# Kernel tuning notes

Measured on AMD Instinct MI355X. Metric: run time of the kernel, lower is better.

The kernel has to match this reference:

```python
import jax, jax.numpy as jnp
import numpy as np

H = 512

def setup_inputs() -> dict:
    key = jax.random.key(0)
    k1, k2, k3, k4, k5 = jax.random.split(key, 5)
    S, B = 2048, 64
    stdv = 1.0 / np.sqrt(H)
    sent_batch = jax.random.normal(k1, (S, B, H), dtype=jnp.float32)
    mean_sent_batch = jax.random.normal(k2, (B, H), dtype=jnp.float32)
    batch_mask = jnp.ones((S, B), dtype=jnp.float32)
    W = jax.random.uniform(k3, (H, H), minval=-stdv, maxval=stdv, dtype=jnp.float32)
    W_h = jax.random.uniform(k4, (H, H), minval=-stdv, maxval=stdv, dtype=jnp.float32)
    context = jax.random.uniform(k5, (H,), minval=-stdv, maxval=stdv, dtype=jnp.float32)
    return {"sent_batch": sent_batch, "mean_sent_batch": mean_sent_batch,
            "batch_mask": batch_mask, "W": W, "W_h": W_h, "context": context}


def reference(sent_batch, mean_sent_batch, batch_mask, W, W_h, context):
    # masked inputs, moved to batch-major: (B, S, H)
    r = (batch_mask[:, :, None] * sent_batch).transpose(1, 0, 2)
    WY = jnp.einsum('bsh,hk->bsk', r, W)                 # (B, S, H)
    WR = mean_sent_batch @ W_h                            # (B, H)
    M = jnp.tanh(WY + WR[:, None, :])                     # (B, S, H)
    scores = jnp.einsum('bsh,h->bs', M, context)          # (B, S)
    alpha = jax.nn.softmax(scores, axis=1)                # softmax over seq_len
    out = jnp.einsum('bs,bsh->bh', alpha, r)              # (B, H)
    return out
```

## Files before the change

kernel.cpp:

```cpp
#include <hip/hip_runtime.h>
#include <hip/hip_bf16.h>
#include <stdint.h>

#define H 512
#define SEQ 2048
#define BATCH 64
#define BH (BATCH * H)

typedef float f32x4 __attribute__((ext_vector_type(4)));
typedef short bf16x8 __attribute__((ext_vector_type(8)));

__device__ __forceinline__ unsigned short f2bf(float f) {
    unsigned int u = __float_as_uint(f);
    u += 0x7fff + ((u >> 16) & 1);
    return (unsigned short)(u >> 16);
}

__global__ __launch_bounds__(256) void prep_kernel(const float* __restrict__ W,
                                                   const float* __restrict__ mean_sb,
                                                   const float* __restrict__ W_h,
                                                   unsigned short* __restrict__ W_t,
                                                   float* __restrict__ WR) {
    int bid = blockIdx.x;
    int tid = threadIdx.x;
    if (bid < 1024) {
        int idx = bid * 256 + tid;
        int k = idx >> 9;
        int n = idx & 511;
        W_t[n * H + k] = f2bf(W[k * H + n]);
    } else {
        int b = bid - 1024;
        float a0 = 0.f, a1 = 0.f;
        for (int k = 0; k < H; ++k) {
            float m = mean_sb[b * H + k];
            a0 += m * W_h[k * H + tid];
            a1 += m * W_h[k * H + tid + 256];
        }
        WR[b * H + tid] = a0;
        WR[b * H + tid + 256] = a1;
    }
}

__global__ __launch_bounds__(256) void scores_kernel(const float* __restrict__ sent,
                                                     const float* __restrict__ mask,
                                                     const unsigned short* __restrict__ W_t,
                                                     const float* __restrict__ WR,
                                                     const float* __restrict__ ctx,
                                                     float* __restrict__ scores) {
    __shared__ uint4 A_lds[64 * 64];
    const int b = blockIdx.y;
    const int s0 = blockIdx.x * 64;
    const int tid = threadIdx.x;
    const int wave = tid >> 6;
    const int lane = tid & 63;
    const int lg = lane >> 4;
    const int ln = lane & 15;

    #pragma unroll 4
    for (int pass = 0; pass < 16; ++pass) {
        int row = pass * 4 + wave;
        int c = lane;
        const float* src = sent + (size_t)(s0 + row) * BH + b * H + c * 8;
        float4 f0 = *(const float4*)src;
        float4 f1 = *(const float4*)(src + 4);
        float m = mask[(s0 + row) * BATCH + b];
        union { unsigned short h[8]; uint4 v; } u;
        u.h[0] = f2bf(f0.x * m); u.h[1] = f2bf(f0.y * m);
        u.h[2] = f2bf(f0.z * m); u.h[3] = f2bf(f0.w * m);
        u.h[4] = f2bf(f1.x * m); u.h[5] = f2bf(f1.y * m);
        u.h[6] = f2bf(f1.z * m); u.h[7] = f2bf(f1.w * m);
        A_lds[row * 64 + (c ^ (row & 7))] = u.v;
    }
    __syncthreads();

    float p[4][4];
    #pragma unroll
    for (int m = 0; m < 4; ++m)
        #pragma unroll
        for (int r = 0; r < 4; ++r) p[m][r] = 0.f;

    const int n_wave = wave * 128;

    #pragma unroll 1
    for (int half = 0; half < 2; ++half) {
        const int n0 = n_wave + half * 64;
        f32x4 acc[4][4];
        #pragma unroll
        for (int m = 0; m < 4; ++m)
            #pragma unroll
            for (int q = 0; q < 4; ++q) acc[m][q] = (f32x4){0.f, 0.f, 0.f, 0.f};

        int arow[4], arowx[4];
        const unsigned short* wbase[4];
        #pragma unroll
        for (int m = 0; m < 4; ++m) {
            int row = m * 16 + ln;
            arow[m] = row * 64;
            arowx[m] = row & 7;
        }
        #pragma unroll
        for (int q = 0; q < 4; ++q)
            wbase[q] = W_t + (size_t)(n0 + q * 16 + ln) * H + lg * 8;

        #pragma unroll 2
        for (int ks = 0; ks < 16; ++ks) {
            bf16x8 a[4], bq[4];
            #pragma unroll
            for (int m = 0; m < 4; ++m) {
                uint4 raw = A_lds[arow[m] + ((4 * ks + lg) ^ arowx[m])];
                union { uint4 v; bf16x8 f; } uu; uu.v = raw;
                a[m] = uu.f;
            }
            #pragma unroll
            for (int q = 0; q < 4; ++q)
                bq[q] = *(const bf16x8*)(wbase[q] + ks * 32);
            #pragma unroll
            for (int m = 0; m < 4; ++m)
                #pragma unroll
                for (int q = 0; q < 4; ++q)
                    acc[m][q] = __builtin_amdgcn_mfma_f32_16x16x32_bf16(a[m], bq[q], acc[m][q], 0, 0, 0);
        }

        #pragma unroll
        for (int q = 0; q < 4; ++q) {
            int n = n0 + q * 16 + ln;
            float wr = WR[b * H + n];
            float cx = ctx[n];
            #pragma unroll
            for (int m = 0; m < 4; ++m)
                #pragma unroll
                for (int r = 0; r < 4; ++r) {
                    float x = acc[m][q][r] + wr;
                    float e = __expf(2.0f * x);
                    p[m][r] += cx * (1.0f - 2.0f * __builtin_amdgcn_rcpf(e + 1.0f));
                }
        }
    }

    #pragma unroll
    for (int m = 0; m < 4; ++m)
        #pragma unroll
        for (int r = 0; r < 4; ++r) {
            float v = p[m][r];
            v += __shfl_xor(v, 1, 16);
            v += __shfl_xor(v, 2, 16);
            v += __shfl_xor(v, 4, 16);
            v += __shfl_xor(v, 8, 16);
            p[m][r] = v;
        }

    __syncthreads();
    float* sp = (float*)A_lds;
    if (ln == 0) {
        #pragma unroll
        for (int m = 0; m < 4; ++m)
            #pragma unroll
            for (int r = 0; r < 4; ++r)
                sp[wave * 64 + m * 16 + lg * 4 + r] = p[m][r];
    }
    __syncthreads();
    if (tid < 64) {
        float v = sp[tid] + sp[64 + tid] + sp[128 + tid] + sp[192 + tid];
        scores[b * SEQ + s0 + tid] = v;
    }
}

__global__ __launch_bounds__(256) void softmax_kernel(const float* __restrict__ scores,
                                                      float* __restrict__ alpha) {
    __shared__ float red[8];
    int b = blockIdx.x, tid = threadIdx.x;
    const float* srow = scores + b * SEQ;
    float4 v0 = *(const float4*)(srow + tid * 8);
    float4 v1 = *(const float4*)(srow + tid * 8 + 4);
    float mx = fmaxf(fmaxf(fmaxf(v0.x, v0.y), fmaxf(v0.z, v0.w)),
                     fmaxf(fmaxf(v1.x, v1.y), fmaxf(v1.z, v1.w)));
    #pragma unroll
    for (int m = 1; m <= 32; m <<= 1) mx = fmaxf(mx, __shfl_xor(mx, m, 64));
    int wave = tid >> 6, lane = tid & 63;
    if (lane == 0) red[wave] = mx;
    __syncthreads();
    mx = fmaxf(fmaxf(red[0], red[1]), fmaxf(red[2], red[3]));
    float e[8];
    e[0] = __expf(v0.x - mx); e[1] = __expf(v0.y - mx);
    e[2] = __expf(v0.z - mx); e[3] = __expf(v0.w - mx);
    e[4] = __expf(v1.x - mx); e[5] = __expf(v1.y - mx);
    e[6] = __expf(v1.z - mx); e[7] = __expf(v1.w - mx);
    float sum = ((e[0] + e[1]) + (e[2] + e[3])) + ((e[4] + e[5]) + (e[6] + e[7]));
    #pragma unroll
    for (int m = 1; m <= 32; m <<= 1) sum += __shfl_xor(sum, m, 64);
    if (lane == 0) red[4 + wave] = sum;
    __syncthreads();
    float inv = 1.0f / (((red[4] + red[5]) + (red[6] + red[7])));
    float4 o0 = {e[0] * inv, e[1] * inv, e[2] * inv, e[3] * inv};
    float4 o1 = {e[4] * inv, e[5] * inv, e[6] * inv, e[7] * inv};
    *(float4*)(alpha + b * SEQ + tid * 8) = o0;
    *(float4*)(alpha + b * SEQ + tid * 8 + 4) = o1;
}

__global__ __launch_bounds__(256) void wsum_kernel(const float* __restrict__ sent,
                                                   const float* __restrict__ mask,
                                                   const float* __restrict__ alpha,
                                                   float* __restrict__ out) {
    int b = blockIdx.y;
    int chunk = blockIdx.x;
    int tid = threadIdx.x;
    int h = tid * 2;
    float a0 = 0.f, a1 = 0.f;
    int s_base = chunk * 128;
    #pragma unroll 4
    for (int i = 0; i < 128; ++i) {
        int s = s_base + i;
        float am = alpha[b * SEQ + s] * mask[s * BATCH + b];
        const float* sp = sent + (size_t)s * BH + b * H + h;
        float2 v = *(const float2*)sp;
        a0 += am * v.x;
        a1 += am * v.y;
    }
    atomicAdd(&out[b * H + h], a0);
    atomicAdd(&out[b * H + h + 1], a1);
}

extern "C" void kernel_launch(void* const* d_in, const int* in_sizes, int n_in,
                              void* d_out, int out_size, void* d_ws, size_t ws_size,
                              hipStream_t stream) {
    const float* sent    = (const float*)d_in[0];
    const float* mean_sb = (const float*)d_in[1];
    const float* mask    = (const float*)d_in[2];
    const float* W       = (const float*)d_in[3];
    const float* W_h     = (const float*)d_in[4];
    const float* ctx     = (const float*)d_in[5];
    float* out = (float*)d_out;

    char* ws = (char*)d_ws;
    unsigned short* W_t = (unsigned short*)(ws);
    float* WR           = (float*)(ws + 524288);
    float* scores       = (float*)(ws + 655360);
    float* alpha        = (float*)(ws + 1179648);

    hipMemsetAsync(d_out, 0, (size_t)out_size * sizeof(float), stream);
    prep_kernel<<<1088, 256, 0, stream>>>(W, mean_sb, W_h, W_t, WR);
    scores_kernel<<<dim3(32, 64), 256, 0, stream>>>(sent, mask, W_t, WR, ctx, scores);
    softmax_kernel<<<64, 256, 0, stream>>>(scores, alpha);
    wsum_kernel<<<dim3(16, 64), 256, 0, stream>>>(sent, mask, alpha, out);
}
```

Before: 571.0 us.

## Pre-swizzle W into MFMA fragment layout and widen scores blocks to eight waves

The prep kernel now writes W as bf16 in the exact per-lane MFMA B-fragment order, so each B load in the scores kernel is one coalesced 16-byte load instead of a strided row read. The scores kernel moves to 512 threads with eight waves, each covering 64 output columns in a single pass, which removes the two-half loop and adds parallelism per block. The mask multiply moves into the softmax output, and wsum switches to float4 loads with two sequence rows interleaved per block and twice as many blocks. The cost is more atomics in wsum and a more complex index mapping in prep.

```diff
diff --git a/kernel.cpp b/kernel.cpp
--- a/kernel.cpp
+++ b/kernel.cpp
@@ -19,18 +19,27 @@
 __global__ __launch_bounds__(256) void prep_kernel(const float* __restrict__ W,
                                                    const float* __restrict__ mean_sb,
                                                    const float* __restrict__ W_h,
-                                                   unsigned short* __restrict__ W_t,
+                                                   uint4* __restrict__ Wf,
                                                    float* __restrict__ WR) {
     int bid = blockIdx.x;
     int tid = threadIdx.x;
-    if (bid < 1024) {
-        int idx = bid * 256 + tid;
-        int k = idx >> 9;
-        int n = idx & 511;
-        W_t[n * H + k] = f2bf(W[k * H + n]);
+    if (bid < 128) {
+        int c = bid * 256 + tid;
+        int lane = c & 63;
+        int ks = (c >> 6) & 15;
+        int t = c >> 10;
+        int lg = lane >> 4, ln = lane & 15;
+        int n = t * 16 + ln;
+        int k0 = ks * 32 + lg * 8;
+        union { unsigned short h[8]; uint4 v; } u;
+        #pragma unroll
+        for (int j = 0; j < 8; ++j)
+            u.h[j] = f2bf(W[(size_t)(k0 + j) * H + n]);
+        Wf[c] = u.v;
     } else {
-        int b = bid - 1024;
+        int b = bid - 128;
         float a0 = 0.f, a1 = 0.f;
+        #pragma unroll 4
         for (int k = 0; k < H; ++k) {
             float m = mean_sb[b * H + k];
             a0 += m * W_h[k * H + tid];
@@ -41,12 +50,12 @@
     }
 }
 
-__global__ __launch_bounds__(256) void scores_kernel(const float* __restrict__ sent,
-                                                     const float* __restrict__ mask,
-                                                     const unsigned short* __restrict__ W_t,
-                                                     const float* __restrict__ WR,
-                                                     const float* __restrict__ ctx,
-                                                     float* __restrict__ scores) {
+__global__ __launch_bounds__(512, 4) void scores_kernel(const float* __restrict__ sent,
+                                                        const float* __restrict__ mask,
+                                                        const uint4* __restrict__ Wf,
+                                                        const float* __restrict__ WR,
+                                                        const float* __restrict__ ctx,
+                                                        float* __restrict__ scores) {
     __shared__ uint4 A_lds[64 * 64];
     const int b = blockIdx.y;
     const int s0 = blockIdx.x * 64;
@@ -56,11 +65,10 @@
     const int lg = lane >> 4;
     const int ln = lane & 15;
 
-    #pragma unroll 4
-    for (int pass = 0; pass < 16; ++pass) {
-        int row = pass * 4 + wave;
-        int c = lane;
-        const float* src = sent + (size_t)(s0 + row) * BH + b * H + c * 8;
+    #pragma unroll
+    for (int pass = 0; pass < 8; ++pass) {
+        int row = pass * 8 + wave;
+        const float* src = sent + (size_t)(s0 + row) * BH + b * H + lane * 8;
         float4 f0 = *(const float4*)src;
         float4 f1 = *(const float4*)(src + 4);
         float m = mask[(s0 + row) * BATCH + b];
@@ -69,72 +77,66 @@
         u.h[2] = f2bf(f0.z * m); u.h[3] = f2bf(f0.w * m);
         u.h[4] = f2bf(f1.x * m); u.h[5] = f2bf(f1.y * m);
         u.h[6] = f2bf(f1.z * m); u.h[7] = f2bf(f1.w * m);
-        A_lds[row * 64 + (c ^ (row & 7))] = u.v;
-    }
-    __syncthreads();
-
-    float p[4][4];
+        A_lds[row * 64 + (lane ^ (row & 7))] = u.v;
+    }
+    __syncthreads();
+
+    f32x4 acc[4][4];
     #pragma unroll
     for (int m = 0; m < 4; ++m)
         #pragma unroll
-        for (int r = 0; r < 4; ++r) p[m][r] = 0.f;
-
-    const int n_wave = wave * 128;
-
-    #pragma unroll 1
-    for (int half = 0; half < 2; ++half) {
-        const int n0 = n_wave + half * 64;
-        f32x4 acc[4][4];
+        for (int q = 0; q < 4; ++q) acc[m][q] = (f32x4){0.f, 0.f, 0.f, 0.f};
+
+    int arow[4], arx[4];
+    #pragma unroll
+    for (int m = 0; m < 4; ++m) {
+        int row = m * 16 + ln;
+        arow[m] = row * 64;
+        arx[m] = row & 7;
+    }
+    const uint4* Bp = Wf + (size_t)wave * 4096 + lane;
+
+    #pragma unroll 2
+    for (int ks = 0; ks < 16; ++ks) {
+        bf16x8 a[4], bq[4];
+        #pragma unroll
+        for (int m = 0; m < 4; ++m) {
+            uint4 raw = A_lds[arow[m] + ((4 * ks + lg) ^ arx[m])];
+            union { uint4 v; bf16x8 f; } uu; uu.v = raw;
+            a[m] = uu.f;
+        }
+        #pragma unroll
+        for (int q = 0; q < 4; ++q) {
+            uint4 raw = Bp[q * 1024 + ks * 64];
+            union { uint4 v; bf16x8 f; } uu; uu.v = raw;
+            bq[q] = uu.f;
+        }
         #pragma unroll
         for (int m = 0; m < 4; ++m)
             #pragma unroll
-            for (int q = 0; q < 4; ++q) acc[m][q] = (f32x4){0.f, 0.f, 0.f, 0.f};
-
-        int arow[4], arowx[4];
-        const unsigned short* wbase[4];
-        #pragma unroll
-        for (int m = 0; m < 4; ++m) {
-            int row = m * 16 + ln;
-            arow[m] = row * 64;
-            arowx[m] = row & 7;
-        }
-        #pragma unroll
-        for (int q = 0; q < 4; ++q)
-            wbase[q] = W_t + (size_t)(n0 + q * 16 + ln) * H + lg * 8;
-
-        #pragma unroll 2
-        for (int ks = 0; ks < 16; ++ks) {
-            bf16x8 a[4], bq[4];
+            for (int q = 0; q < 4; ++q)
+                acc[m][q] = __builtin_amdgcn_mfma_f32_16x16x32_bf16(a[m], bq[q], acc[m][q], 0, 0, 0);
+    }
+
+    float p[4][4];
+    #pragma unroll
+    for (int m = 0; m < 4; ++m)
+        #pragma unroll
+        for (int r = 0; r < 4; ++r) p[m][r] = 0.f;
+
+    #pragma unroll
+    for (int q = 0; q < 4; ++q) {
+        int n = wave * 64 + q * 16 + ln;
+        float wr = WR[b * H + n];
+        float cx = ctx[n];
+        #pragma unroll
+        for (int m = 0; m < 4; ++m)
             #pragma unroll
-            for (int m = 0; m < 4; ++m) {
-                uint4 raw = A_lds[arow[m] + ((4 * ks + lg) ^ arowx[m])];
-                union { uint4 v; bf16x8 f; } uu; uu.v = raw;
-                a[m] = uu.f;
+            for (int r = 0; r < 4; ++r) {
+                float x = acc[m][q][r] + wr;
+                float e = __expf(2.0f * x);
+                p[m][r] += cx * (1.0f - 2.0f * __builtin_amdgcn_rcpf(e + 1.0f));
             }
-            #pragma unroll
-            for (int q = 0; q < 4; ++q)
-                bq[q] = *(const bf16x8*)(wbase[q] + ks * 32);
-            #pragma unroll
-            for (int m = 0; m < 4; ++m)
-                #pragma unroll
-                for (int q = 0; q < 4; ++q)
-                    acc[m][q] = __builtin_amdgcn_mfma_f32_16x16x32_bf16(a[m], bq[q], acc[m][q], 0, 0, 0);
-        }
-
-        #pragma unroll
-        for (int q = 0; q < 4; ++q) {
-            int n = n0 + q * 16 + ln;
-            float wr = WR[b * H + n];
-            float cx = ctx[n];
-            #pragma unroll
-            for (int m = 0; m < 4; ++m)
-                #pragma unroll
-                for (int r = 0; r < 4; ++r) {
-                    float x = acc[m][q][r] + wr;
-                    float e = __expf(2.0f * x);
-                    p[m][r] += cx * (1.0f - 2.0f * __builtin_amdgcn_rcpf(e + 1.0f));
-                }
-        }
     }
 
     #pragma unroll
@@ -160,13 +162,16 @@
     }
     __syncthreads();
     if (tid < 64) {
-        float v = sp[tid] + sp[64 + tid] + sp[128 + tid] + sp[192 + tid];
+        float v = 0.f;
+        #pragma unroll
+        for (int w = 0; w < 8; ++w) v += sp[w * 64 + tid];
         scores[b * SEQ + s0 + tid] = v;
     }
 }
 
 __global__ __launch_bounds__(256) void softmax_kernel(const float* __restrict__ scores,
-                                                      float* __restrict__ alpha) {
+                                                      const float* __restrict__ mask,
+                                                      float* __restrict__ alphap) {
     __shared__ float red[8];
     int b = blockIdx.x, tid = threadIdx.x;
     const float* srow = scores + b * SEQ;
@@ -191,33 +196,42 @@
     if (lane == 0) red[4 + wave] = sum;
     __syncthreads();
     float inv = 1.0f / (((red[4] + red[5]) + (red[6] + red[7])));
-    float4 o0 = {e[0] * inv, e[1] * inv, e[2] * inv, e[3] * inv};
-    float4 o1 = {e[4] * inv, e[5] * inv, e[6] * inv, e[7] * inv};
-    *(float4*)(alpha + b * SEQ + tid * 8) = o0;
-    *(float4*)(alpha + b * SEQ + tid * 8 + 4) = o1;
+    int s8 = tid * 8;
+    float4 o0, o1;
+    o0.x = e[0] * inv * mask[(s8 + 0) * BATCH + b];
+    o0.y = e[1] * inv * mask[(s8 + 1) * BATCH + b];
+    o0.z = e[2] * inv * mask[(s8 + 2) * BATCH + b];
+    o0.w = e[3] * inv * mask[(s8 + 3) * BATCH + b];
+    o1.x = e[4] * inv * mask[(s8 + 4) * BATCH + b];
+    o1.y = e[5] * inv * mask[(s8 + 5) * BATCH + b];
+    o1.z = e[6] * inv * mask[(s8 + 6) * BATCH + b];
+    o1.w = e[7] * inv * mask[(s8 + 7) * BATCH + b];
+    *(float4*)(alphap + b * SEQ + s8) = o0;
+    *(float4*)(alphap + b * SEQ + s8 + 4) = o1;
 }
 
 __global__ __launch_bounds__(256) void wsum_kernel(const float* __restrict__ sent,
-                                                   const float* __restrict__ mask,
-                                                   const float* __restrict__ alpha,
+                                                   const float* __restrict__ alphap,
                                                    float* __restrict__ out) {
     int b = blockIdx.y;
     int chunk = blockIdx.x;
     int tid = threadIdx.x;
-    int h = tid * 2;
-    float a0 = 0.f, a1 = 0.f;
-    int s_base = chunk * 128;
+    int sub = tid >> 7;
+    int hq = (tid & 127) * 4;
+    int sbase = chunk * 64 + sub;
+    f32x4 acc = {0.f, 0.f, 0.f, 0.f};
     #pragma unroll 4
-    for (int i = 0; i < 128; ++i) {
-        int s = s_base + i;
-        float am = alpha[b * SEQ + s] * mask[s * BATCH + b];
-        const float* sp = sent + (size_t)s * BH + b * H + h;
-        float2 v = *(const float2*)sp;
-        a0 += am * v.x;
-        a1 += am * v.y;
-    }
-    atomicAdd(&out[b * H + h], a0);
-    atomicAdd(&out[b * H + h + 1], a1);
+    for (int i = 0; i < 32; ++i) {
+        int s = sbase + i * 2;
+        float am = alphap[b * SEQ + s];
+        float4 v = *(const float4*)(sent + (size_t)s * BH + b * H + hq);
+        acc.x += am * v.x; acc.y += am * v.y;
+        acc.z += am * v.z; acc.w += am * v.w;
+    }
+    atomicAdd(&out[b * H + hq + 0], acc.x);
+    atomicAdd(&out[b * H + hq + 1], acc.y);
+    atomicAdd(&out[b * H + hq + 2], acc.z);
+    atomicAdd(&out[b * H + hq + 3], acc.w);
 }
 
 extern "C" void kernel_launch(void* const* d_in, const int* in_sizes, int n_in,
@@ -232,14 +246,14 @@
     float* out = (float*)d_out;
 
     char* ws = (char*)d_ws;
-    unsigned short* W_t = (unsigned short*)(ws);
-    float* WR           = (float*)(ws + 524288);
-    float* scores       = (float*)(ws + 655360);
-    float* alpha        = (float*)(ws + 1179648);
+    uint4* Wf    = (uint4*)(ws);
+    float* WR    = (float*)(ws + 524288);
+    float* scores = (float*)(ws + 655360);
+    float* alphap = (float*)(ws + 1179648);
 
     hipMemsetAsync(d_out, 0, (size_t)out_size * sizeof(float), stream);
-    prep_kernel<<<1088, 256, 0, stream>>>(W, mean_sb, W_h, W_t, WR);
-    scores_kernel<<<dim3(32, 64), 256, 0, stream>>>(sent, mask, W_t, WR, ctx, scores);
-    softmax_kernel<<<64, 256, 0, stream>>>(scores, alpha);
-    wsum_kernel<<<dim3(16, 64), 256, 0, stream>>>(sent, mask, alpha, out);
-}
+    prep_kernel<<<192, 256, 0, stream>>>(W, mean_sb, W_h, Wf, WR);
+    scores_kernel<<<dim3(32, 64), 512, 0, stream>>>(sent, mask, Wf, WR, ctx, scores);
+    softmax_kernel<<<64, 256, 0, stream>>>(scores, mask, alphap);
+    wsum_kernel<<<dim3(32, 64), 256, 0, stream>>>(sent, alphap, out);
+}
```

After: 543.3 us. -4.9%, faster.
